# Performance work log

Measured on AMD Instinct MI355X. Metric: run time of the kernel, lower is better.

The kernel has to match this reference:

```python
import jax, jax.numpy as jnp
import numpy as np

NUM_CAPSULE = 16
DIM_CAPSULE = 64
ROUTINGS = 3
T_EPS = 1e-7


def setup_inputs() -> dict:
    key = jax.random.key(0)
    k1, k2 = jax.random.split(key)
    x = jax.random.normal(k1, (64, 512, 768), dtype=jnp.float32)
    # xavier-normal-ish init for W: [1, input_dim_capsule, num_capsule*dim_capsule]
    fan_in, fan_out = 768, NUM_CAPSULE * DIM_CAPSULE
    std = float(np.sqrt(2.0 / (fan_in + fan_out)))
    W = jax.random.normal(k2, (1, 768, NUM_CAPSULE * DIM_CAPSULE), dtype=jnp.float32) * std
    return {"x": x, "W": W}


def _squash(v, eps=T_EPS):
    # NOTE: this module's 'squash' is pure L2 normalization with eps, not the
    # classic (s^2/(1+s^2)) squash.
    s2 = jnp.sum(v * v, axis=-1, keepdims=True)
    return v / jnp.sqrt(s2 + eps)


def reference(x, W):
    B, In, _ = x.shape
    # u_hat: [B, In, num*dim] -> [B, num, In, dim]
    u = jnp.matmul(x, W).reshape(B, In, NUM_CAPSULE, DIM_CAPSULE).transpose(0, 2, 1, 3)
    b = jnp.zeros((B, NUM_CAPSULE, In), dtype=u.dtype)  # routing logits
    outputs = None
    for i in range(ROUTINGS):
        # torch code softmaxes over the num_capsule axis (after permute dance)
        c = jax.nn.softmax(b, axis=1)  # [B, num, In]
        outputs = _squash(jnp.einsum('bij,bijk->bik', c, u))  # [B, num, dim]
        if i < ROUTINGS - 1:
            b = jnp.einsum('bik,bijk->bij', outputs, u)  # [B, num, In]
    return outputs
```

## Files before the change

### kernel.cpp

```cpp
#include <hip/hip_runtime.h>
#include <hip/hip_cooperative_groups.h>
#include <hip/hip_bf16.h>
#include <stdint.h>

namespace cg = cooperative_groups;

#define BATCH 64
#define IN_CAPS 512
#define NCAP 16
#define DCAP 64
#define GN (NCAP * DCAP)
#define GM (BATCH * IN_CAPS)
#define GK 768
#define NUM_CU 256

typedef __bf16 bf16;
typedef __attribute__((ext_vector_type(8))) __bf16 bf16x8;
typedef __attribute__((ext_vector_type(4))) float f32x4;

__device__ inline void async16(const bf16* g, bf16* l) {
    __builtin_amdgcn_global_load_lds(
        (__attribute__((address_space(1))) void*)g,
        (__attribute__((address_space(3))) void*)l, 16, 0, 0);
}

__global__ __launch_bounds__(256) void k_convX2(const float* __restrict__ X,
                                                bf16* __restrict__ Xb,
                                                float* __restrict__ XS) {
    __shared__ float ls[GK];
    const int tid = threadIdx.x;
    ls[tid] = 0.f; ls[tid + 256] = 0.f; ls[tid + 512] = 0.f;
    __syncthreads();
    const size_t base = (size_t)blockIdx.x * (32 * GK);
    float acc[3][8] = {};
#pragma unroll
    for (int r = 0; r < 12; ++r) {
        const int off = r * 2048 + tid * 8;
        const f32x4 a0 = *(const f32x4*)(X + base + off);
        const f32x4 a1 = *(const f32x4*)(X + base + off + 4);
        bf16x8 o;
        o[0] = (bf16)a0[0]; o[1] = (bf16)a0[1]; o[2] = (bf16)a0[2]; o[3] = (bf16)a0[3];
        o[4] = (bf16)a1[0]; o[5] = (bf16)a1[1]; o[6] = (bf16)a1[2]; o[7] = (bf16)a1[3];
        *(bf16x8*)(Xb + base + off) = o;
        const int g = r % 3;
        acc[g][0] += a0[0]; acc[g][1] += a0[1];
        acc[g][2] += a0[2]; acc[g][3] += a0[3];
        acc[g][4] += a1[0]; acc[g][5] += a1[1];
        acc[g][6] += a1[2]; acc[g][7] += a1[3];
    }
    if (XS != nullptr) {
#pragma unroll
        for (int g = 0; g < 3; ++g) {
            const int cg2 = (g == 1) ? 512 : (g == 2) ? 256 : 0;
            const int kb = (tid * 8 + cg2) % GK;
#pragma unroll
            for (int j = 0; j < 8; ++j) atomicAdd(&ls[kb + j], acc[g][j]);
        }
        __syncthreads();
        const int bidx = blockIdx.x >> 4;
        atomicAdd(&XS[(size_t)bidx * GK + tid],       ls[tid]);
        atomicAdd(&XS[(size_t)bidx * GK + tid + 256], ls[tid + 256]);
        atomicAdd(&XS[(size_t)bidx * GK + tid + 512], ls[tid + 512]);
    }
}

__global__ void k_transW(const float* __restrict__ W, bf16* __restrict__ Wt,
                         float* __restrict__ XS) {
    __shared__ bf16 t[32][33];
    const int k0 = blockIdx.x * 32;
    const int n0 = blockIdx.y * 32;
    const int tx = threadIdx.x, ty = threadIdx.y;
    if (XS != nullptr) {
        const int gid = (blockIdx.y * gridDim.x + blockIdx.x) * 256 + ty * 32 + tx;
        if (gid < BATCH * GK) XS[gid] = 0.f;
    }
#pragma unroll
    for (int r = 0; r < 4; ++r)
        t[ty + r * 8][tx] = (bf16)W[(size_t)(k0 + ty + r * 8) * GN + n0 + tx];
    __syncthreads();
#pragma unroll
    for (int r = 0; r < 4; ++r)
        Wt[(size_t)(n0 + ty + r * 8) * GK + k0 + tx] = t[tx][ty + r * 8];
}

__global__ __launch_bounds__(256) void k_out1(const float* __restrict__ XS,
                                              const float* __restrict__ W,
                                              float* __restrict__ O1) {
    __shared__ float xs[4][GK];
    __shared__ float red[4][4][64];
    const int cap = blockIdx.x & 15;
    const int bg = blockIdx.x >> 4;
    const int tid = threadIdx.x;
    const int k = tid & 63, kq = tid >> 6;
#pragma unroll
    for (int bb = 0; bb < 4; ++bb) {
        const size_t b = (size_t)(bg * 4 + bb);
        xs[bb][tid]       = XS[b * GK + tid];
        xs[bb][tid + 256] = XS[b * GK + tid + 256];
        xs[bb][tid + 512] = XS[b * GK + tid + 512];
    }
    __syncthreads();
    float acc4[4] = {0.f, 0.f, 0.f, 0.f};
    const float* wp = W + (size_t)(kq * 192) * GN + cap * 64 + k;
#pragma unroll 4
    for (int kk = 0; kk < 192; ++kk) {
        const float w = wp[(size_t)kk * GN];
        const int kx = kq * 192 + kk;
        acc4[0] += xs[0][kx] * w;
        acc4[1] += xs[1][kx] * w;
        acc4[2] += xs[2][kx] * w;
        acc4[3] += xs[3][kx] * w;
    }
#pragma unroll
    for (int bb = 0; bb < 4; ++bb) red[bb][kq][k] = acc4[bb];
    __syncthreads();
    if (tid < 64) {
#pragma unroll
        for (int bb = 0; bb < 4; ++bb) {
            float s = (red[bb][0][tid] + red[bb][1][tid] +
                       red[bb][2][tid] + red[bb][3][tid]) * 0.0625f;
            float ss = s * s;
#pragma unroll
            for (int off = 32; off >= 1; off >>= 1) ss += __shfl_xor(ss, off);
            O1[((size_t)(bg * 4 + bb) * NCAP + cap) * DCAP + tid] =
                s * rsqrtf(ss + 1e-7f);
        }
    }
}

__global__ __launch_bounds__(256) void k_gemm_async(const bf16* __restrict__ Xb,
                                                    const bf16* __restrict__ Wt,
                                                    const float* __restrict__ O1,
                                                    bf16* __restrict__ U,
                                                    float* __restrict__ BL) {
    __shared__ bf16 sA[128 * 32];
    __shared__ bf16 sB[128 * 32];

    const int tid = threadIdx.x;
    const int lane = tid & 63;
    const int wave = tid >> 6;
    const int wm = wave >> 1, wn = wave & 1;
    const int m0 = blockIdx.x * 128;
    const int n0 = blockIdx.y * 128;

    const int c0 = wave * 2, c1 = wave * 2 + 1;
    const int rl = lane >> 2, cl = (lane & 3) * 8;
    const bf16* gA0 = Xb + (size_t)(m0 + c0 * 16 + rl) * GK + cl;
    const bf16* gA1 = Xb + (size_t)(m0 + c1 * 16 + rl) * GK + cl;
    const bf16* gB0 = Wt + (size_t)(n0 + c0 * 16 + rl) * GK + cl;
    const bf16* gB1 = Wt + (size_t)(n0 + c1 * 16 + rl) * GK + cl;
    bf16* lA0 = sA + c0 * 512;
    bf16* lA1 = sA + c1 * 512;
    bf16* lB0 = sB + c0 * 512;
    bf16* lB1 = sB + c1 * 512;

    f32x4 acc[4][4] = {};
    const int fr = lane & 15;
    const int fq = lane >> 4;

    for (int kt = 0; kt < GK / 32; ++kt) {
        __syncthreads();
        async16(gA0, lA0);
        async16(gA1, lA1);
        async16(gB0, lB0);
        async16(gB1, lB1);
        gA0 += 32; gA1 += 32; gB0 += 32; gB1 += 32;
        __syncthreads();

        bf16x8 af[4], bfr[4];
#pragma unroll
        for (int mi = 0; mi < 4; ++mi)
            af[mi] = *(const bf16x8*)(sA + (wm * 64 + mi * 16 + fr) * 32 + fq * 8);
#pragma unroll
        for (int ni = 0; ni < 4; ++ni)
            bfr[ni] = *(const bf16x8*)(sB + (wn * 64 + ni * 16 + fr) * 32 + fq * 8);
#pragma unroll
        for (int mi = 0; mi < 4; ++mi)
#pragma unroll
            for (int ni = 0; ni < 4; ++ni)
                acc[mi][ni] = __builtin_amdgcn_mfma_f32_16x16x32_bf16(
                    af[mi], bfr[ni], acc[mi][ni], 0, 0, 0);
    }

#pragma unroll
    for (int mi = 0; mi < 4; ++mi) {
#pragma unroll
        for (int ni = 0; ni < 4; ++ni) {
#pragma unroll
            for (int r = 0; r < 4; ++r) {
                const int m = m0 + wm * 64 + mi * 16 + fq * 4 + r;
                const int n = n0 + wn * 64 + ni * 16 + fr;
                const int bb = m >> 9, j = m & 511;
                const int ci = n >> 6, k = n & 63;
                U[(((size_t)(bb * NCAP + ci)) * IN_CAPS + j) * DCAP + k] =
                    (bf16)acc[mi][ni][r];
            }
        }
    }

    if (O1 != nullptr) {
        const int b = m0 >> 9;
        const int cap = (n0 >> 6) + wn;
        float o1v[4];
#pragma unroll
        for (int ni = 0; ni < 4; ++ni)
            o1v[ni] = O1[(size_t)b * GN + n0 + wn * 64 + ni * 16 + fr];
#pragma unroll
        for (int mi = 0; mi < 4; ++mi) {
#pragma unroll
            for (int r = 0; r < 4; ++r) {
                float p = o1v[0] * acc[mi][0][r] + o1v[1] * acc[mi][1][r] +
                          o1v[2] * acc[mi][2][r] + o1v[3] * acc[mi][3][r];
                p += __shfl_xor(p, 1);
                p += __shfl_xor(p, 2);
                p += __shfl_xor(p, 4);
                p += __shfl_xor(p, 8);
                if (fr == 0) {
                    const int j = (m0 & 511) + wm * 64 + mi * 16 + fq * 4 + r;
                    BL[((size_t)(b * NCAP + cap)) * IN_CAPS + j] = p;
                }
            }
        }
    }
}

__global__ __launch_bounds__(256) void k_gemm_inline(const float* __restrict__ X,
                                                     const bf16* __restrict__ Wt,
                                                     bf16* __restrict__ U) {
    __shared__ bf16 sA[128 * 32];
    __shared__ bf16 sB[128 * 32];
    const int tid = threadIdx.x;
    const int lane = tid & 63;
    const int wave = tid >> 6;
    const int wm = wave >> 1, wn = wave & 1;
    const int m0 = blockIdx.x * 128;
    const int n0 = blockIdx.y * 128;
    const int srow = tid >> 2;
    const int scol = (tid & 3) * 8;
    f32x4 acc[4][4] = {};
    const int fr = lane & 15;
    const int fq = lane >> 4;
    for (int kt = 0; kt < GK / 32; ++kt) {
        const int kb = kt * 32;
        bf16x8 a0, a1, b0, b1;
        {
            const float* p = X + (size_t)(m0 + srow) * GK + kb + scol;
            const f32x4 x0 = *(const f32x4*)p, x1 = *(const f32x4*)(p + 4);
            const float* q = X + (size_t)(m0 + srow + 64) * GK + kb + scol;
            const f32x4 y0 = *(const f32x4*)q, y1 = *(const f32x4*)(q + 4);
#pragma unroll
            for (int c = 0; c < 4; ++c) {
                a0[c] = (bf16)x0[c]; a0[c + 4] = (bf16)x1[c];
                a1[c] = (bf16)y0[c]; a1[c + 4] = (bf16)y1[c];
            }
        }
        b0 = *(const bf16x8*)(Wt + (size_t)(n0 + srow) * GK + kb + scol);
        b1 = *(const bf16x8*)(Wt + (size_t)(n0 + srow + 64) * GK + kb + scol);
        __syncthreads();
        *(bf16x8*)(sA + srow * 32 + scol) = a0;
        *(bf16x8*)(sA + (srow + 64) * 32 + scol) = a1;
        *(bf16x8*)(sB + srow * 32 + scol) = b0;
        *(bf16x8*)(sB + (srow + 64) * 32 + scol) = b1;
        __syncthreads();
        bf16x8 af[4], bfr[4];
#pragma unroll
        for (int mi = 0; mi < 4; ++mi)
            af[mi] = *(const bf16x8*)(sA + (wm * 64 + mi * 16 + fr) * 32 + fq * 8);
#pragma unroll
        for (int ni = 0; ni < 4; ++ni)
            bfr[ni] = *(const bf16x8*)(sB + (wn * 64 + ni * 16 + fr) * 32 + fq * 8);
#pragma unroll
        for (int mi = 0; mi < 4; ++mi)
#pragma unroll
            for (int ni = 0; ni < 4; ++ni)
                acc[mi][ni] = __builtin_amdgcn_mfma_f32_16x16x32_bf16(
                    af[mi], bfr[ni], acc[mi][ni], 0, 0, 0);
    }
#pragma unroll
    for (int mi = 0; mi < 4; ++mi) {
#pragma unroll
        for (int ni = 0; ni < 4; ++ni) {
#pragma unroll
            for (int r = 0; r < 4; ++r) {
                const int m = m0 + wm * 64 + mi * 16 + fq * 4 + r;
                const int n = n0 + wn * 64 + ni * 16 + fr;
                const int bb = m >> 9, j = m & 511;
                const int ci = n >> 6, k = n & 63;
                U[(((size_t)(bb * NCAP + ci)) * IN_CAPS + j) * DCAP + k] =
                    (bf16)acc[mi][ni][r];
            }
        }
    }
}

__global__ __launch_bounds__(256, 4) void k_route_coop(const bf16* __restrict__ U,
                                                       const float* __restrict__ BLin,
                                                       float* __restrict__ BLtmp,
                                                       float* __restrict__ OutC) {
    __shared__ float sc[IN_CAPS];
    __shared__ float red2[4][64];
    __shared__ float sout[64];
    const int bi = blockIdx.x;
    const int b = bi >> 4, cap = bi & 15;
    const int tid = threadIdx.x;
    const int lane = tid & 63;
    const int wave = tid >> 6;
    const int g = tid & 7;
    const int jr = tid >> 3;
    const size_t ubase = (size_t)bi * IN_CAPS * DCAP;

#pragma unroll
    for (int h = 0; h < 2; ++h) {
        const int j = tid + h * 256;
        const float* p = BLin + (size_t)b * NCAP * IN_CAPS + j;
        float mx = -1e30f;
#pragma unroll
        for (int i = 0; i < 16; ++i) mx = fmaxf(mx, p[(size_t)i * IN_CAPS]);
        float s = 0.f;
#pragma unroll
        for (int i = 0; i < 16; ++i) s += __expf(p[(size_t)i * IN_CAPS] - mx);
        sc[j] = __expf(p[(size_t)cap * IN_CAPS] - mx) / s;
    }
    __syncthreads();

    bf16x8 ur[16];
    float acc[8] = {};
#pragma unroll
    for (int it = 0; it < 16; ++it) {
        ur[it] = *(const bf16x8*)(U + ubase + (size_t)it * 2048 + tid * 8);
        const float cv = sc[it * 32 + jr];
#pragma unroll
        for (int c = 0; c < 8; ++c) acc[c] += cv * (float)ur[it][c];
    }
#pragma unroll
    for (int c = 0; c < 8; ++c) {
        acc[c] += __shfl_xor(acc[c], 8);
        acc[c] += __shfl_xor(acc[c], 16);
        acc[c] += __shfl_xor(acc[c], 32);
    }
    if ((lane >> 3) == 0) {
#pragma unroll
        for (int c = 0; c < 8; ++c) red2[wave][lane * 8 + c] = acc[c];
    }
    __syncthreads();
    if (tid < 64) {
        float s = red2[0][tid] + red2[1][tid] + red2[2][tid] + red2[3][tid];
        float ss = s * s;
#pragma unroll
        for (int off = 32; off >= 1; off >>= 1) ss += __shfl_xor(ss, off);
        sout[tid] = s * rsqrtf(ss + 1e-7f);
    }
    __syncthreads();

    {
        const f32x4 o0 = *(const f32x4*)(sout + g * 8);
        const f32x4 o1 = *(const f32x4*)(sout + g * 8 + 4);
#pragma unroll
        for (int it = 0; it < 16; ++it) {
            const bf16x8 v = ur[it];
            float p = o0[0] * (float)v[0] + o0[1] * (float)v[1] +
                      o0[2] * (float)v[2] + o0[3] * (float)v[3] +
                      o1[0] * (float)v[4] + o1[1] * (float)v[5] +
                      o1[2] * (float)v[6] + o1[3] * (float)v[7];
            p += __shfl_xor(p, 1);
            p += __shfl_xor(p, 2);
            p += __shfl_xor(p, 4);
            if (g == 0)
                BLtmp[((size_t)(b * NCAP + cap)) * IN_CAPS + it * 32 + jr] = p;
        }
    }

    __threadfence();
    cg::this_grid().sync();

#pragma unroll
    for (int h = 0; h < 2; ++h) {
        const int j = tid + h * 256;
        const float* p = BLtmp + (size_t)b * NCAP * IN_CAPS + j;
        float mx = -1e30f;
#pragma unroll
        for (int i = 0; i < 16; ++i) mx = fmaxf(mx, p[(size_t)i * IN_CAPS]);
        float s = 0.f;
#pragma unroll
        for (int i = 0; i < 16; ++i) s += __expf(p[(size_t)i * IN_CAPS] - mx);
        sc[j] = __expf(p[(size_t)cap * IN_CAPS] - mx) / s;
    }
    __syncthreads();

    float acc2[8] = {};
#pragma unroll
    for (int it = 0; it < 16; ++it) {
        const float cv = sc[it * 32 + jr];
#pragma unroll
        for (int c = 0; c < 8; ++c) acc2[c] += cv * (float)ur[it][c];
    }
#pragma unroll
    for (int c = 0; c < 8; ++c) {
        acc2[c] += __shfl_xor(acc2[c], 8);
        acc2[c] += __shfl_xor(acc2[c], 16);
        acc2[c] += __shfl_xor(acc2[c], 32);
    }
    if ((lane >> 3) == 0) {
#pragma unroll
        for (int c = 0; c < 8; ++c) red2[wave][lane * 8 + c] = acc2[c];
    }
    __syncthreads();
    if (tid < 64) {
        float s = red2[0][tid] + red2[1][tid] + red2[2][tid] + red2[3][tid];
        float ss = s * s;
#pragma unroll
        for (int off = 32; off >= 1; off >>= 1) ss += __shfl_xor(ss, off);
        OutC[(size_t)bi * DCAP + tid] = s * rsqrtf(ss + 1e-7f);
    }
}

__global__ __launch_bounds__(256) void k_route(const bf16* __restrict__ U,
                                               float* __restrict__ BL,
                                               float* __restrict__ OutC,
                                               int mode) {
    __shared__ float sc[IN_CAPS];
    __shared__ float red2[4][64];
    __shared__ float sout[64];
    const int bi = blockIdx.x;
    const int b = bi >> 4, cap = bi & 15;
    const int tid = threadIdx.x;
    const int lane = tid & 63;
    const int wave = tid >> 6;
    const size_t ubase = (size_t)bi * IN_CAPS * DCAP;

    if (mode == 0) {
        sc[tid] = 0.0625f;
        sc[tid + 256] = 0.0625f;
    } else {
#pragma unroll
        for (int h = 0; h < 2; ++h) {
            const int j = tid + h * 256;
            const float* p = BL + (size_t)b * NCAP * IN_CAPS + j;
            float v[16], mx = -1e30f;
#pragma unroll
            for (int i = 0; i < 16; ++i) {
                v[i] = p[(size_t)i * IN_CAPS];
                mx = fmaxf(mx, v[i]);
            }
            float s = 0.f;
#pragma unroll
            for (int i = 0; i < 16; ++i) s += __expf(v[i] - mx);
            sc[j] = __expf(v[cap] - mx) / s;
        }
    }
    __syncthreads();

    const int g = tid & 7;
    const int jr = tid >> 3;

    float acc[8] = {};
#pragma unroll
    for (int it = 0; it < 16; ++it) {
        const int j = it * 32 + jr;
        const bf16x8 v = *(const bf16x8*)(U + ubase + (size_t)it * 2048 + tid * 8);
        const float cv = sc[j];
#pragma unroll
        for (int c = 0; c < 8; ++c) acc[c] += cv * (float)v[c];
    }
#pragma unroll
    for (int c = 0; c < 8; ++c) {
        acc[c] += __shfl_xor(acc[c], 8);
        acc[c] += __shfl_xor(acc[c], 16);
        acc[c] += __shfl_xor(acc[c], 32);
    }
    if ((lane >> 3) == 0) {
#pragma unroll
        for (int c = 0; c < 8; ++c) red2[wave][lane * 8 + c] = acc[c];
    }
    __syncthreads();

    if (tid < 64) {
        float s = red2[0][tid] + red2[1][tid] + red2[2][tid] + red2[3][tid];
        float ss = s * s;
#pragma unroll
        for (int off = 32; off >= 1; off >>= 1) ss += __shfl_xor(ss, off);
        const float val = s * rsqrtf(ss + 1e-7f);
        sout[tid] = val;
        if (mode == 2) OutC[(size_t)bi * DCAP + tid] = val;
    }
    if (mode == 2) return;
    __syncthreads();

    const f32x4 o0 = *(const f32x4*)(sout + g * 8);
    const f32x4 o1 = *(const f32x4*)(sout + g * 8 + 4);
#pragma unroll
    for (int it = 0; it < 16; ++it) {
        const int j = it * 32 + jr;
        const bf16x8 v = *(const bf16x8*)(U + ubase + (size_t)it * 2048 + tid * 8);
        float p = o0[0] * (float)v[0] + o0[1] * (float)v[1] +
                  o0[2] * (float)v[2] + o0[3] * (float)v[3] +
                  o1[0] * (float)v[4] + o1[1] * (float)v[5] +
                  o1[2] * (float)v[6] + o1[3] * (float)v[7];
        p += __shfl_xor(p, 1);
        p += __shfl_xor(p, 2);
        p += __shfl_xor(p, 4);
        if (g == 0) BL[((size_t)b * NCAP + cap) * IN_CAPS + j] = p;
    }
}

extern "C" void kernel_launch(void* const* d_in, const int* in_sizes, int n_in,
                              void* d_out, int out_size, void* d_ws, size_t ws_size,
                              hipStream_t stream) {
    const float* X = (const float*)d_in[0];
    const float* W = (const float*)d_in[1];
    float* OutC = (float*)d_out;

    const size_t u_bytes = (size_t)BATCH * NCAP * IN_CAPS * DCAP * sizeof(bf16);
    const size_t xb_bytes = (size_t)GM * GK * sizeof(bf16);
    const size_t wt_bytes = (size_t)GN * GK * sizeof(bf16);
    const size_t bl_bytes = (size_t)BATCH * NCAP * IN_CAPS * sizeof(float);
    const size_t xs_bytes = (size_t)BATCH * GK * sizeof(float);
    const size_t o1_bytes = (size_t)BATCH * GN * sizeof(float);
    char* ws = (char*)d_ws;

    const size_t need_full = u_bytes + xb_bytes + wt_bytes + bl_bytes + xs_bytes + o1_bytes;
    const size_t need_async = u_bytes + xb_bytes + wt_bytes + bl_bytes;
    const size_t need_small = u_bytes + wt_bytes + bl_bytes;

    bf16* U = (bf16*)ws;

    if (ws_size >= need_full) {
        bf16* Xb = (bf16*)(ws + u_bytes);
        bf16* Wt = (bf16*)(ws + u_bytes + xb_bytes);
        float* BL = (float*)(ws + u_bytes + xb_bytes + wt_bytes);
        float* XS = (float*)(ws + u_bytes + xb_bytes + wt_bytes + bl_bytes);
        float* O1 = (float*)(ws + u_bytes + xb_bytes + wt_bytes + bl_bytes + xs_bytes);
        k_transW<<<dim3(GK / 32, GN / 32), dim3(32, 8), 0, stream>>>(W, Wt, XS);
        k_convX2<<<GM / 32, 256, 0, stream>>>(X, Xb, XS);
        k_out1<<<256, 256, 0, stream>>>(XS, W, O1);
        k_gemm_async<<<dim3(GM / 128, GN / 128), 256, 0, stream>>>(Xb, Wt, O1, U, BL);

        float* BLtmp = (float*)Xb;
        int maxBlk = 0;
        hipError_t oe = hipOccupancyMaxActiveBlocksPerMultiprocessor(
            &maxBlk, k_route_coop, 256, 0);
        bool coop_ok = false;
        if (oe == hipSuccess && maxBlk >= 4) {
            const bf16* Uc = U;
            const float* BLc = BL;
            void* kargs[] = {(void*)&Uc, (void*)&BLc, (void*)&BLtmp, (void*)&OutC};
            hipError_t le = hipLaunchCooperativeKernel(
                k_route_coop, dim3(BATCH * NCAP), dim3(256), kargs, 0, stream);
            coop_ok = (le == hipSuccess);
        }
        if (!coop_ok) {
            k_route<<<BATCH * NCAP, 256, 0, stream>>>(U, BL, OutC, 1);
            k_route<<<BATCH * NCAP, 256, 0, stream>>>(U, BL, OutC, 2);
        }
    } else if (ws_size >= need_async) {
        bf16* Xb = (bf16*)(ws + u_bytes);
        bf16* Wt = (bf16*)(ws + u_bytes + xb_bytes);
        float* BL = (float*)(ws + u_bytes + xb_bytes + wt_bytes);
        k_transW<<<dim3(GK / 32, GN / 32), dim3(32, 8), 0, stream>>>(W, Wt, nullptr);
        k_convX2<<<GM / 32, 256, 0, stream>>>(X, Xb, nullptr);
        k_gemm_async<<<dim3(GM / 128, GN / 128), 256, 0, stream>>>(Xb, Wt, nullptr, U, BL);
        k_route<<<BATCH * NCAP, 256, 0, stream>>>(U, BL, OutC, 0);
        k_route<<<BATCH * NCAP, 256, 0, stream>>>(U, BL, OutC, 1);
        k_route<<<BATCH * NCAP, 256, 0, stream>>>(U, BL, OutC, 2);
    } else if (ws_size >= need_small) {
        bf16* Wt = (bf16*)(ws + u_bytes);
        float* BL = (float*)(ws + u_bytes + wt_bytes);
        k_transW<<<dim3(GK / 32, GN / 32), dim3(32, 8), 0, stream>>>(W, Wt, nullptr);
        k_gemm_inline<<<dim3(GM / 128, GN / 128), 256, 0, stream>>>(X, Wt, U);
        k_route<<<BATCH * NCAP, 256, 0, stream>>>(U, BL, OutC, 0);
        k_route<<<BATCH * NCAP, 256, 0, stream>>>(U, BL, OutC, 1);
        k_route<<<BATCH * NCAP, 256, 0, stream>>>(U, BL, OutC, 2);
    }
}
```

Baseline: 296.6 us.

## Fuse W transpose into X prep, drop atomics and cooperative routing grid sync

The separate W-transpose and X-conversion kernels are merged into one launch that splits its blocks by role. Per-block column sums are written as partial rows that k_out1 reduces, replacing global atomics and the zeroing pass. The GEMM grid becomes 1-D with a swizzled block-to-tile mapping for better cache locality. The cooperative routing kernel with a grid-wide sync is replaced by two ordinary launches: one writes the new logits and one does the final pass. This trades a grid barrier for an extra launch and a re-read of U.

```diff
diff --git a/kernel.cpp b/kernel.cpp
--- a/kernel.cpp
+++ b/kernel.cpp
@@ -1,9 +1,6 @@
 #include <hip/hip_runtime.h>
-#include <hip/hip_cooperative_groups.h>
 #include <hip/hip_bf16.h>
 #include <stdint.h>
-
-namespace cg = cooperative_groups;
 
 #define BATCH 64
 #define IN_CAPS 512
@@ -12,7 +9,6 @@
 #define GN (NCAP * DCAP)
 #define GM (BATCH * IN_CAPS)
 #define GK 768
-#define NUM_CU 256
 
 typedef __bf16 bf16;
 typedef __attribute__((ext_vector_type(8))) __bf16 bf16x8;
@@ -24,56 +20,76 @@
         (__attribute__((address_space(3))) void*)l, 16, 0, 0);
 }
 
-__global__ __launch_bounds__(256) void k_convX2(const float* __restrict__ X,
-                                                bf16* __restrict__ Xb,
-                                                float* __restrict__ XS) {
+__global__ __launch_bounds__(256) void k_prep(const float* __restrict__ X,
+                                              bf16* __restrict__ Xb,
+                                              float* __restrict__ XSP,
+                                              const float* __restrict__ W,
+                                              bf16* __restrict__ Wt) {
     __shared__ float ls[GK];
+    __shared__ bf16 tsh[32][33];
     const int tid = threadIdx.x;
-    ls[tid] = 0.f; ls[tid + 256] = 0.f; ls[tid + 512] = 0.f;
-    __syncthreads();
-    const size_t base = (size_t)blockIdx.x * (32 * GK);
-    float acc[3][8] = {};
-#pragma unroll
-    for (int r = 0; r < 12; ++r) {
-        const int off = r * 2048 + tid * 8;
-        const f32x4 a0 = *(const f32x4*)(X + base + off);
-        const f32x4 a1 = *(const f32x4*)(X + base + off + 4);
-        bf16x8 o;
-        o[0] = (bf16)a0[0]; o[1] = (bf16)a0[1]; o[2] = (bf16)a0[2]; o[3] = (bf16)a0[3];
-        o[4] = (bf16)a1[0]; o[5] = (bf16)a1[1]; o[6] = (bf16)a1[2]; o[7] = (bf16)a1[3];
-        *(bf16x8*)(Xb + base + off) = o;
-        const int g = r % 3;
-        acc[g][0] += a0[0]; acc[g][1] += a0[1];
-        acc[g][2] += a0[2]; acc[g][3] += a0[3];
-        acc[g][4] += a1[0]; acc[g][5] += a1[1];
-        acc[g][6] += a1[2]; acc[g][7] += a1[3];
-    }
-    if (XS != nullptr) {
+
+    if (blockIdx.x < 1024) {
+        ls[tid] = 0.f; ls[tid + 256] = 0.f; ls[tid + 512] = 0.f;
+        __syncthreads();
+        const size_t base = (size_t)blockIdx.x * (32 * GK);
+        float acc[3][8] = {};
+#pragma unroll
+        for (int r = 0; r < 12; ++r) {
+            const int off = r * 2048 + tid * 8;
+            const f32x4 a0 = *(const f32x4*)(X + base + off);
+            const f32x4 a1 = *(const f32x4*)(X + base + off + 4);
+            bf16x8 o;
+            o[0] = (bf16)a0[0]; o[1] = (bf16)a0[1]; o[2] = (bf16)a0[2]; o[3] = (bf16)a0[3];
+            o[4] = (bf16)a1[0]; o[5] = (bf16)a1[1]; o[6] = (bf16)a1[2]; o[7] = (bf16)a1[3];
+            *(bf16x8*)(Xb + base + off) = o;
+            const int g = r % 3;
+            acc[g][0] += a0[0]; acc[g][1] += a0[1];
+            acc[g][2] += a0[2]; acc[g][3] += a0[3];
+            acc[g][4] += a1[0]; acc[g][5] += a1[1];
+            acc[g][6] += a1[2]; acc[g][7] += a1[3];
+        }
 #pragma unroll
         for (int g = 0; g < 3; ++g) {
-            const int cg2 = (g == 1) ? 512 : (g == 2) ? 256 : 0;
-            const int kb = (tid * 8 + cg2) % GK;
+            const int cg = (g == 1) ? 512 : (g == 2) ? 256 : 0;
+            const int kb = (tid * 8 + cg) % GK;
 #pragma unroll
             for (int j = 0; j < 8; ++j) atomicAdd(&ls[kb + j], acc[g][j]);
         }
         __syncthreads();
-        const int bidx = blockIdx.x >> 4;
-        atomicAdd(&XS[(size_t)bidx * GK + tid],       ls[tid]);
-        atomicAdd(&XS[(size_t)bidx * GK + tid + 256], ls[tid + 256]);
-        atomicAdd(&XS[(size_t)bidx * GK + tid + 512], ls[tid + 512]);
-    }
-}
-
-__global__ void k_transW(const float* __restrict__ W, bf16* __restrict__ Wt,
-                         float* __restrict__ XS) {
+        float* P = XSP + (size_t)blockIdx.x * GK;
+        P[tid] = ls[tid]; P[tid + 256] = ls[tid + 256]; P[tid + 512] = ls[tid + 512];
+    } else {
+        const int t = blockIdx.x - 1024;
+        const int k0 = (t % 24) * 32;
+        const int n0 = (t / 24) * 32;
+        const int tx = tid & 31, ty = tid >> 5;
+#pragma unroll
+        for (int r = 0; r < 4; ++r)
+            tsh[ty + r * 8][tx] = (bf16)W[(size_t)(k0 + ty + r * 8) * GN + n0 + tx];
+        __syncthreads();
+#pragma unroll
+        for (int r = 0; r < 4; ++r)
+            Wt[(size_t)(n0 + ty + r * 8) * GK + k0 + tx] = tsh[tx][ty + r * 8];
+    }
+}
+
+__global__ __launch_bounds__(256) void k_convX(const float* __restrict__ X,
+                                               bf16* __restrict__ Xb) {
+    const size_t i = ((size_t)blockIdx.x * 256 + threadIdx.x) * 8;
+    const f32x4 a = *(const f32x4*)(X + i);
+    const f32x4 b = *(const f32x4*)(X + i + 4);
+    bf16x8 r;
+    r[0] = (bf16)a[0]; r[1] = (bf16)a[1]; r[2] = (bf16)a[2]; r[3] = (bf16)a[3];
+    r[4] = (bf16)b[0]; r[5] = (bf16)b[1]; r[6] = (bf16)b[2]; r[7] = (bf16)b[3];
+    *(bf16x8*)(Xb + i) = r;
+}
+
+__global__ void k_transW(const float* __restrict__ W, bf16* __restrict__ Wt) {
     __shared__ bf16 t[32][33];
     const int k0 = blockIdx.x * 32;
     const int n0 = blockIdx.y * 32;
     const int tx = threadIdx.x, ty = threadIdx.y;
-    if (XS != nullptr) {
-        const int gid = (blockIdx.y * gridDim.x + blockIdx.x) * 256 + ty * 32 + tx;
-        if (gid < BATCH * GK) XS[gid] = 0.f;
-    }
 #pragma unroll
     for (int r = 0; r < 4; ++r)
         t[ty + r * 8][tx] = (bf16)W[(size_t)(k0 + ty + r * 8) * GN + n0 + tx];
@@ -83,7 +99,7 @@
         Wt[(size_t)(n0 + ty + r * 8) * GK + k0 + tx] = t[tx][ty + r * 8];
 }
 
-__global__ __launch_bounds__(256) void k_out1(const float* __restrict__ XS,
+__global__ __launch_bounds__(256) void k_out1(const float* __restrict__ XSP,
                                               const float* __restrict__ W,
                                               float* __restrict__ O1) {
     __shared__ float xs[4][GK];
@@ -94,10 +110,15 @@
     const int k = tid & 63, kq = tid >> 6;
 #pragma unroll
     for (int bb = 0; bb < 4; ++bb) {
-        const size_t b = (size_t)(bg * 4 + bb);
-        xs[bb][tid]       = XS[b * GK + tid];
-        xs[bb][tid + 256] = XS[b * GK + tid + 256];
-        xs[bb][tid + 512] = XS[b * GK + tid + 512];
+        const float* P = XSP + (size_t)(bg * 4 + bb) * 16 * GK;
+        float s0 = 0.f, s1 = 0.f, s2 = 0.f;
+#pragma unroll
+        for (int s = 0; s < 16; ++s) {
+            s0 += P[s * GK + tid];
+            s1 += P[s * GK + tid + 256];
+            s2 += P[s * GK + tid + 512];
+        }
+        xs[bb][tid] = s0; xs[bb][tid + 256] = s1; xs[bb][tid + 512] = s2;
     }
     __syncthreads();
     float acc4[4] = {0.f, 0.f, 0.f, 0.f};
@@ -140,8 +161,10 @@
     const int lane = tid & 63;
     const int wave = tid >> 6;
     const int wm = wave >> 1, wn = wave & 1;
-    const int m0 = blockIdx.x * 128;
-    const int n0 = blockIdx.y * 128;
+    const int bid = blockIdx.x;
+    const int swz = (bid & 7) * 256 + (bid >> 3);
+    const int m0 = (swz >> 3) * 128;
+    const int n0 = (swz & 7) * 128;
 
     const int c0 = wave * 2, c1 = wave * 2 + 1;
     const int rl = lane >> 2, cl = (lane & 3) * 8;
@@ -293,10 +316,9 @@
     }
 }
 
-__global__ __launch_bounds__(256, 4) void k_route_coop(const bf16* __restrict__ U,
-                                                       const float* __restrict__ BLin,
-                                                       float* __restrict__ BLtmp,
-                                                       float* __restrict__ OutC) {
+__global__ void k_route1r(const bf16* __restrict__ U,
+                          const float* __restrict__ BLin,
+                          float* __restrict__ BLout) {
     __shared__ float sc[IN_CAPS];
     __shared__ float red2[4][64];
     __shared__ float sout[64];
@@ -352,65 +374,20 @@
     }
     __syncthreads();
 
-    {
-        const f32x4 o0 = *(const f32x4*)(sout + g * 8);
-        const f32x4 o1 = *(const f32x4*)(sout + g * 8 + 4);
-#pragma unroll
-        for (int it = 0; it < 16; ++it) {
-            const bf16x8 v = ur[it];
-            float p = o0[0] * (float)v[0] + o0[1] * (float)v[1] +
-                      o0[2] * (float)v[2] + o0[3] * (float)v[3] +
-                      o1[0] * (float)v[4] + o1[1] * (float)v[5] +
-                      o1[2] * (float)v[6] + o1[3] * (float)v[7];
-            p += __shfl_xor(p, 1);
-            p += __shfl_xor(p, 2);
-            p += __shfl_xor(p, 4);
-            if (g == 0)
-                BLtmp[((size_t)(b * NCAP + cap)) * IN_CAPS + it * 32 + jr] = p;
-        }
-    }
-
-    __threadfence();
-    cg::this_grid().sync();
-
-#pragma unroll
-    for (int h = 0; h < 2; ++h) {
-        const int j = tid + h * 256;
-        const float* p = BLtmp + (size_t)b * NCAP * IN_CAPS + j;
-        float mx = -1e30f;
-#pragma unroll
-        for (int i = 0; i < 16; ++i) mx = fmaxf(mx, p[(size_t)i * IN_CAPS]);
-        float s = 0.f;
-#pragma unroll
-        for (int i = 0; i < 16; ++i) s += __expf(p[(size_t)i * IN_CAPS] - mx);
-        sc[j] = __expf(p[(size_t)cap * IN_CAPS] - mx) / s;
-    }
-    __syncthreads();
-
-    float acc2[8] = {};
+    const f32x4 o0 = *(const f32x4*)(sout + g * 8);
+    const f32x4 o1 = *(const f32x4*)(sout + g * 8 + 4);
 #pragma unroll
     for (int it = 0; it < 16; ++it) {
-        const float cv = sc[it * 32 + jr];
-#pragma unroll
-        for (int c = 0; c < 8; ++c) acc2[c] += cv * (float)ur[it][c];
-    }
-#pragma unroll
-    for (int c = 0; c < 8; ++c) {
-        acc2[c] += __shfl_xor(acc2[c], 8);
-        acc2[c] += __shfl_xor(acc2[c], 16);
-        acc2[c] += __shfl_xor(acc2[c], 32);
-    }
-    if ((lane >> 3) == 0) {
-#pragma unroll
-        for (int c = 0; c < 8; ++c) red2[wave][lane * 8 + c] = acc2[c];
-    }
-    __syncthreads();
-    if (tid < 64) {
-        float s = red2[0][tid] + red2[1][tid] + red2[2][tid] + red2[3][tid];
-        float ss = s * s;
-#pragma unroll
-        for (int off = 32; off >= 1; off >>= 1) ss += __shfl_xor(ss, off);
-        OutC[(size_t)bi * DCAP + tid] = s * rsqrtf(ss + 1e-7f);
+        const bf16x8 v = ur[it];
+        float p = o0[0] * (float)v[0] + o0[1] * (float)v[1] +
+                  o0[2] * (float)v[2] + o0[3] * (float)v[3] +
+                  o1[0] * (float)v[4] + o1[1] * (float)v[5] +
+                  o1[2] * (float)v[6] + o1[3] * (float)v[7];
+        p += __shfl_xor(p, 1);
+        p += __shfl_xor(p, 2);
+        p += __shfl_xor(p, 4);
+        if (g == 0)
+            BLout[((size_t)(b * NCAP + cap)) * IN_CAPS + it * 32 + jr] = p;
     }
 }
 
@@ -514,11 +491,11 @@
     const size_t xb_bytes = (size_t)GM * GK * sizeof(bf16);
     const size_t wt_bytes = (size_t)GN * GK * sizeof(bf16);
     const size_t bl_bytes = (size_t)BATCH * NCAP * IN_CAPS * sizeof(float);
-    const size_t xs_bytes = (size_t)BATCH * GK * sizeof(float);
+    const size_t xsp_bytes = (size_t)1024 * GK * sizeof(float);
     const size_t o1_bytes = (size_t)BATCH * GN * sizeof(float);
     char* ws = (char*)d_ws;
 
-    const size_t need_full = u_bytes + xb_bytes + wt_bytes + bl_bytes + xs_bytes + o1_bytes;
+    const size_t need_full = u_bytes + xb_bytes + wt_bytes + bl_bytes + xsp_bytes + o1_bytes;
     const size_t need_async = u_bytes + xb_bytes + wt_bytes + bl_bytes;
     const size_t need_small = u_bytes + wt_bytes + bl_bytes;
 
@@ -528,44 +505,29 @@
         bf16* Xb = (bf16*)(ws + u_bytes);
         bf16* Wt = (bf16*)(ws + u_bytes + xb_bytes);
         float* BL = (float*)(ws + u_bytes + xb_bytes + wt_bytes);
-        float* XS = (float*)(ws + u_bytes + xb_bytes + wt_bytes + bl_bytes);
-        float* O1 = (float*)(ws + u_bytes + xb_bytes + wt_bytes + bl_bytes + xs_bytes);
-        k_transW<<<dim3(GK / 32, GN / 32), dim3(32, 8), 0, stream>>>(W, Wt, XS);
-        k_convX2<<<GM / 32, 256, 0, stream>>>(X, Xb, XS);
-        k_out1<<<256, 256, 0, stream>>>(XS, W, O1);
-        k_gemm_async<<<dim3(GM / 128, GN / 128), 256, 0, stream>>>(Xb, Wt, O1, U, BL);
-
+        float* XSP = (float*)(ws + u_bytes + xb_bytes + wt_bytes + bl_bytes);
+        float* O1 = (float*)(ws + u_bytes + xb_bytes + wt_bytes + bl_bytes + xsp_bytes);
         float* BLtmp = (float*)Xb;
-        int maxBlk = 0;
-        hipError_t oe = hipOccupancyMaxActiveBlocksPerMultiprocessor(
-            &maxBlk, k_route_coop, 256, 0);
-        bool coop_ok = false;
-        if (oe == hipSuccess && maxBlk >= 4) {
-            const bf16* Uc = U;
-            const float* BLc = BL;
-            void* kargs[] = {(void*)&Uc, (void*)&BLc, (void*)&BLtmp, (void*)&OutC};
-            hipError_t le = hipLaunchCooperativeKernel(
-                k_route_coop, dim3(BATCH * NCAP), dim3(256), kargs, 0, stream);
-            coop_ok = (le == hipSuccess);
-        }
-        if (!coop_ok) {
-            k_route<<<BATCH * NCAP, 256, 0, stream>>>(U, BL, OutC, 1);
-            k_route<<<BATCH * NCAP, 256, 0, stream>>>(U, BL, OutC, 2);
-        }
+
+        k_prep<<<1024 + 768, 256, 0, stream>>>(X, Xb, XSP, W, Wt);
+        k_out1<<<256, 256, 0, stream>>>(XSP, W, O1);
+        k_gemm_async<<<2048, 256, 0, stream>>>(Xb, Wt, O1, U, BL);
+        k_route1r<<<BATCH * NCAP, 256, 0, stream>>>(U, BL, BLtmp);
+        k_route<<<BATCH * NCAP, 256, 0, stream>>>(U, BLtmp, OutC, 2);
     } else if (ws_size >= need_async) {
         bf16* Xb = (bf16*)(ws + u_bytes);
         bf16* Wt = (bf16*)(ws + u_bytes + xb_bytes);
         float* BL = (float*)(ws + u_bytes + xb_bytes + wt_bytes);
-        k_transW<<<dim3(GK / 32, GN / 32), dim3(32, 8), 0, stream>>>(W, Wt, nullptr);
-        k_convX2<<<GM / 32, 256, 0, stream>>>(X, Xb, nullptr);
-        k_gemm_async<<<dim3(GM / 128, GN / 128), 256, 0, stream>>>(Xb, Wt, nullptr, U, BL);
+        k_transW<<<dim3(GK / 32, GN / 32), dim3(32, 8), 0, stream>>>(W, Wt);
+        k_convX<<<GM * GK / (256 * 8), 256, 0, stream>>>(X, Xb);
+        k_gemm_async<<<2048, 256, 0, stream>>>(Xb, Wt, nullptr, U, BL);
         k_route<<<BATCH * NCAP, 256, 0, stream>>>(U, BL, OutC, 0);
         k_route<<<BATCH * NCAP, 256, 0, stream>>>(U, BL, OutC, 1);
         k_route<<<BATCH * NCAP, 256, 0, stream>>>(U, BL, OutC, 2);
     } else if (ws_size >= need_small) {
         bf16* Wt = (bf16*)(ws + u_bytes);
         float* BL = (float*)(ws + u_bytes + wt_bytes);
-        k_transW<<<dim3(GK / 32, GN / 32), dim3(32, 8), 0, stream>>>(W, Wt, nullptr);
+        k_transW<<<dim3(GK / 32, GN / 32), dim3(32, 8), 0, stream>>>(W, Wt);
         k_gemm_inline<<<dim3(GM / 128, GN / 128), 256, 0, stream>>>(X, Wt, U);
         k_route<<<BATCH * NCAP, 256, 0, stream>>>(U, BL, OutC, 0);
         k_route<<<BATCH * NCAP, 256, 0, stream>>>(U, BL, OutC, 1);
```

Result: slower. 324.1 us (+9.3%).
